# Kernel optimization log

Measured on AMD Instinct MI355X. Metric: run time of the kernel, lower is better.

The kernel has to match this reference:

```python
import jax, jax.numpy as jnp
import numpy as np

CHAIN = (0, 1, 2)
BETA, GAMMA, REG = 1.0, 500.0, 0.2


def _rbf(x, y, V, l):
    """exp(- sum_{V,d}(x-y)^2 / (d*V*V)) + l*I, via the |x|^2+|y|^2-2xy trick.
    x, y: (N, V, d)."""
    N, _, d = x.shape
    xf = x.reshape(N, -1)
    yf = y.reshape(N, -1)
    sq = (jnp.sum(xf * xf, axis=1)[:, None]
          + jnp.sum(yf * yf, axis=1)[None, :]
          - 2.0 * (xf @ yf.T))  # (N, N) sum of squared diffs over V*d
    k = jnp.exp(-sq / (d * V * V))
    if l != 0.0:
        k = k + l * jnp.eye(N, dtype=x.dtype)
    return k


def _trprod(A, B):
    # trace(A @ B) without materializing the product
    return jnp.sum(A * B.T)


def _cmmd(Q, P, endo, exo, l):
    N = Q.shape[0]
    P = jnp.broadcast_to(P, Q.shape)  # handles std_norm with d=1
    endo = list(endo)
    Ve = len(endo)
    qe, pe = Q[:, endo, :], P[:, endo, :]
    Lqq = _rbf(qe, qe, Ve, 0.0)
    Lpp = _rbf(pe, pe, Ve, 0.0)
    Lqp = _rbf(qe, pe, Ve, 0.0)
    if len(exo) == 0:
        # conditional matrices are all-ones -> trace(L @ J) = sum(L)
        return (jnp.sum(Lqq) + jnp.sum(Lpp) - 2.0 * jnp.sum(Lqp)) / (N * N)
    exo = list(exo)
    Vx = len(exo)
    qx, px = Q[:, exo, :], P[:, exo, :]
    Kq_inv = jnp.linalg.inv(_rbf(qx, qx, Vx, l))
    Kp_inv = jnp.linalg.inv(_rbf(px, px, Vx, l))
    Cqq = Kq_inv @ _rbf(qx, qx, Vx, 0.0) @ Kq_inv
    Cpp = Kp_inv @ _rbf(px, px, Vx, 0.0) @ Kp_inv
    Cqp = Kp_inv @ _rbf(px, qx, Vx, 0.0) @ Kq_inv  # inv(Kpp) @ Kpq @ inv(Kqq)
    return (_trprod(Lqq, Cqq) + _trprod(Lpp, Cpp)
            - 2.0 * _trprod(Lqp, Cqp)) / (N * N)


def setup_inputs() -> dict:
    key = jax.random.key(0)
    ks = jax.random.split(key, 5)
    N, V, d, D = 4096, 8, 32, 256
    return {
        "x": jax.random.normal(ks[0], (N, D), dtype=jnp.float32),
        "z": jax.random.normal(ks[1], (N, V, d), dtype=jnp.float32),
        "zz": jax.random.normal(ks[2], (N, V, d), dtype=jnp.float32),
        "xx": jax.random.normal(ks[3], (N, D), dtype=jnp.float32),
        "std_norm": jax.random.normal(ks[4], (N, V, 1), dtype=jnp.float32),
    }


def reference(x, z, zz, xx, std_norm):
    all_endo = tuple(range(z.shape[1]))
    mmd = BETA * _cmmd(z, std_norm, all_endo, (), 0.1)
    mmd = mmd + GAMMA * (
        _cmmd(zz, z, (CHAIN[0],), (CHAIN[1],), REG)
        + _cmmd(zz, z, (CHAIN[1],), (CHAIN[2],), REG)
        + _cmmd(zz, z, (CHAIN[0],), (CHAIN[2],), REG))
    nll = jnp.sum((xx - x) ** 2) / (2.0 * x.shape[0])
    return mmd, nll
```

## Files before the change

### kernel.cpp

```cpp
#include <hip/hip_runtime.h>
#include <math.h>

#define NN 4096
#define DD 256
#define NV 8
#define VD 32
#define NB 128
#define NBLK (NN/NB)
#define NTRI (NBLK*(NBLK+1)/2)

#define RMAP(ty,u) ((ty)*4 + (((u)>>2)<<6) + ((u)&3))
#define CMAP(tx,v) ((tx)*4 + (((v)>>2)<<6) + ((v)&3))

typedef __attribute__((ext_vector_type(8))) short bf16x8;
typedef __attribute__((ext_vector_type(4))) float f32x4;

#define AS1(p) ((const __attribute__((address_space(1))) void*)(p))
#define AS3(p) ((__attribute__((address_space(3))) void*)(p))

__device__ __forceinline__ void stage16(const ushort* g, ushort* l){
  __builtin_amdgcn_global_load_lds(AS1(g), AS3(l), 16, 0, 0);
}

__device__ __forceinline__ ushort f2bf(float x){
  uint u = __float_as_uint(x);
  u += 0x7FFFu + ((u >> 16) & 1u);
  return (ushort)(u >> 16);
}
__device__ __forceinline__ float bf2f(ushort h){ return __uint_as_float(((uint)h) << 16); }

__device__ __forceinline__ void tri_map(int p, int& bi, int& bj){
  int b = (int)((sqrtf(8.0f * (float)p + 1.0f) - 1.0f) * 0.5f);
  while ((b + 1) * (b + 2) / 2 <= p) b++;
  while (b * (b + 1) / 2 > p) b--;
  bi = b; bj = p - b * (b + 1) / 2;
}

__device__ __forceinline__ void block_atomic_add(float v, float* red, float* dst){
  #pragma unroll
  for (int off = 32; off > 0; off >>= 1) v += __shfl_down(v, off, 64);
  const int lane = threadIdx.x & 63;
  const int w = threadIdx.x >> 6;
  if (lane == 0) red[w] = v;
  __syncthreads();
  if (threadIdx.x == 0) atomicAdd(dst, red[0] + red[1] + red[2] + red[3]);
  __syncthreads();
}

#define STAGE_AB(tAp, tBp, kk) do { \
  _Pragma("unroll") \
  for (int p_ = 0; p_ < 2; p_++){ \
    const int row_ = p_*64 + (t >> 2); \
    const int lo_ = row_*32 + sch; \
    stage16(Ah + (size_t)(r0 + row_) * NN + (kk) + sch, (tAp) + lo_); \
    stage16(Bh + (size_t)(c0 + row_) * NN + (kk) + sch, (tBp) + lo_); \
  } } while(0)

#define MFMA_STEP(tAp, tBp) do { \
  bf16x8 ah_[4], bh_[4]; \
  _Pragma("unroll") \
  for (int i_ = 0; i_ < 4; i_++){ \
    ah_[i_] = *(const bf16x8*)&(tAp)[(wr*64 + i_*16 + lm)*32 + quad*8]; \
    bh_[i_] = *(const bf16x8*)&(tBp)[(wc*64 + i_*16 + lm)*32 + quad*8]; \
  } \
  _Pragma("unroll") \
  for (int i_ = 0; i_ < 4; i_++) \
    _Pragma("unroll") \
    for (int j_ = 0; j_ < 4; j_++) \
      acc[i_][j_] = __builtin_amdgcn_mfma_f32_16x16x32_bf16(ah_[i_], bh_[j_], acc[i_][j_], 0, 0, 0); \
  } while(0)

#define PIPE_WAIT_BAR(N) do { \
  asm volatile("s_waitcnt vmcnt(" #N ")" ::: "memory"); \
  __builtin_amdgcn_s_barrier(); \
  } while(0)
#define PIPE_BAR() do { \
  asm volatile("" ::: "memory"); \
  __builtin_amdgcn_s_barrier(); \
  asm volatile("" ::: "memory"); \
  } while(0)

#define PIPE_MAIN_LOOP() do { \
  STAGE_AB(shb + 0*8192, shb + 0*8192 + 4096, 0); \
  STAGE_AB(shb + 1*8192, shb + 1*8192 + 4096, 32); \
  STAGE_AB(shb + 2*8192, shb + 2*8192 + 4096, 64); \
  int cur = 0; \
  _Pragma("unroll 1") \
  for (int step = 0; step < 125; step++){ \
    ushort* tA = shb + cur*8192; ushort* tB = tA + 4096; \
    PIPE_WAIT_BAR(8); \
    MFMA_STEP(tA, tB); \
    PIPE_BAR(); \
    STAGE_AB(tA, tB, (step+3)*32); \
    cur++; if (cur == 3) cur = 0; \
  } \
  { ushort* tA = shb + cur*8192; ushort* tB = tA + 4096; \
    PIPE_WAIT_BAR(8); MFMA_STEP(tA, tB); cur++; if (cur == 3) cur = 0; } \
  { ushort* tA = shb + cur*8192; ushort* tB = tA + 4096; \
    PIPE_WAIT_BAR(4); MFMA_STEP(tA, tB); cur++; if (cur == 3) cur = 0; } \
  { ushort* tA = shb + cur*8192; ushort* tB = tA + 4096; \
    PIPE_WAIT_BAR(0); MFMA_STEP(tA, tB); } \
  } while(0)

__global__ void k_zero(float* p, int n){
  int i = blockIdx.x * blockDim.x + threadIdx.x;
  if (i < n) p[i] = 0.f;
}

__global__ void k_norms(const float* __restrict__ z, const float* __restrict__ zz,
                        const float* __restrict__ stdn,
                        float* __restrict__ stdsq, float* __restrict__ zrs,
                        float* __restrict__ nzz, float* __restrict__ nz8){
  int t = blockIdx.x * blockDim.x + threadIdx.x;
  if (t >= NN * NV) return;
  int i = t / NV, v = t % NV;
  const float* zp  = z  + (size_t)i * DD + v * VD;
  const float* zzp = zz + (size_t)i * DD + v * VD;
  float s1 = 0.f, s2 = 0.f, s2z = 0.f;
  #pragma unroll
  for (int k = 0; k < VD; k++){
    float a = zp[k];  s1 += a; s2 += a * a;
    float b = zzp[k]; s2z += b * b;
  }
  zrs[(size_t)i * NV + v] = s1;
  nz8[(size_t)v * NN + i] = s2;
  nzz[(size_t)v * NN + i] = s2z;
  if (v == 0){
    float s = 0.f;
    #pragma unroll
    for (int u = 0; u < NV; u++){ float a = stdn[(size_t)i * NV + u]; s += a * a; }
    stdsq[i] = s;
  }
}

__global__ void k_rownorm(const float* __restrict__ nz8, float* __restrict__ nrmz){
  int i = blockIdx.x * blockDim.x + threadIdx.x;
  if (i < NN){
    float s = 0.f;
    #pragma unroll
    for (int v = 0; v < NV; v++) s += nz8[(size_t)v * NN + i];
    nrmz[i] = s;
  }
}

__global__ __launch_bounds__(256) void k_nll(const float* __restrict__ x,
                                             const float* __restrict__ xx,
                                             float* __restrict__ slots){
  __shared__ float red[4];
  float s = 0.f;
  const int total = NN * DD;
  for (int i = (blockIdx.x * 256 + threadIdx.x) * 4; i < total; i += gridDim.x * 256 * 4){
    float4 a = *(const float4*)(x + i);
    float4 b = *(const float4*)(xx + i);
    float d0 = b.x - a.x, d1 = b.y - a.y, d2 = b.z - a.z, d3 = b.w - a.w;
    s += d0*d0 + d1*d1 + d2*d2 + d3*d3;
  }
  block_atomic_add(s, red, slots + 3);
}

__global__ __launch_bounds__(256) void k_sqq(const float* __restrict__ z,
                                             const float* __restrict__ nrm,
                                             float* __restrict__ slots){
  __shared__ float Xr[128 * 33];
  __shared__ float Xc[128 * 33];
  __shared__ float red[4];
  int bi, bj; tri_map(blockIdx.x, bi, bj);
  const int r0 = bi * 128, c0 = bj * 128;
  const float wgt = (bi != bj) ? 2.f : 1.f;
  const int t = threadIdx.x;
  const int tx = t & 15, ty = t >> 4;
  const int lrow = t >> 1, lh = t & 1;
  float acc[8][8];
  #pragma unroll
  for (int u = 0; u < 8; u++)
    #pragma unroll
    for (int v = 0; v < 8; v++) acc[u][v] = 0.f;
  for (int ks = 0; ks < DD; ks += 32){
    const float* pr = z + (size_t)(r0 + lrow) * DD + ks + lh * 16;
    const float* pc = z + (size_t)(c0 + lrow) * DD + ks + lh * 16;
    float* dr = &Xr[lrow * 33 + lh * 16];
    float* dc = &Xc[lrow * 33 + lh * 16];
    #pragma unroll
    for (int u = 0; u < 4; u++){
      float4 a = ((const float4*)pr)[u];
      dr[4*u+0] = a.x; dr[4*u+1] = a.y; dr[4*u+2] = a.z; dr[4*u+3] = a.w;
      float4 b = ((const float4*)pc)[u];
      dc[4*u+0] = b.x; dc[4*u+1] = b.y; dc[4*u+2] = b.z; dc[4*u+3] = b.w;
    }
    __syncthreads();
    #pragma unroll
    for (int kk = 0; kk < 32; kk++){
      float a[8], b[8];
      #pragma unroll
      for (int u = 0; u < 8; u++) a[u] = Xr[RMAP(ty,u)*33 + kk];
      #pragma unroll
      for (int v = 0; v < 8; v++) b[v] = Xc[CMAP(tx,v)*33 + kk];
      #pragma unroll
      for (int u = 0; u < 8; u++)
        #pragma unroll
        for (int v = 0; v < 8; v++) acc[u][v] += a[u] * b[v];
    }
    __syncthreads();
  }
  float s = 0.f;
  #pragma unroll 1
  for (int u = 0; u < 8; u++){
    const float ni = nrm[r0 + RMAP(ty,u)];
    #pragma unroll 1
    for (int v = 0; v < 8; v++)
      s += __expf(-(ni + nrm[c0 + CMAP(tx,v)] - 2.f * acc[u][v]) * (1.f/2048.f));
  }
  block_atomic_add(s * wgt, red, slots + 0);
}

__global__ __launch_bounds__(256) void k_spp_sqp(const float* __restrict__ stdn,
                                                 const float* __restrict__ stdsq,
                                                 const float* __restrict__ zrs,
                                                 const float* __restrict__ nrmz,
                                                 float* __restrict__ slots){
  __shared__ float sI[128*9], sJ[128*9], zI[128*9];
  __shared__ float qI[128], qJ[128], nI[128];
  __shared__ float red[4];
  const int r0 = blockIdx.y * 128, c0 = blockIdx.x * 128;
  const int t = threadIdx.x;
  if (t < 128){
    #pragma unroll
    for (int v = 0; v < 8; v++){
      sI[t*9+v] = stdn[(size_t)(r0+t)*NV + v];
      sJ[t*9+v] = stdn[(size_t)(c0+t)*NV + v];
      zI[t*9+v] = zrs[(size_t)(r0+t)*NV + v];
    }
    qI[t] = stdsq[r0+t]; qJ[t] = stdsq[c0+t]; nI[t] = nrmz[r0+t];
  }
  __syncthreads();
  const int tx = t & 15, ty = t >> 4;
  float spp = 0.f, sqp = 0.f;
  #pragma unroll 1
  for (int u = 0; u < 8; u++){
    int i = ty + 16*u;
    #pragma unroll 1
    for (int v = 0; v < 8; v++){
      int j = tx + 16*v;
      float dpp = 0.f, dqp = 0.f;
      #pragma unroll
      for (int k = 0; k < 8; k++){
        float sj = sJ[j*9+k];
        dpp += sI[i*9+k] * sj;
        dqp += zI[i*9+k] * sj;
      }
      spp += __expf(-(qI[i] + qJ[j] - 2.f*dpp) * (1.f/64.f));
      sqp += __expf(-(nI[i] + 32.f*qJ[j] - 2.f*dqp) * (1.f/2048.f));
    }
  }
  block_atomic_add(spp, red, slots + 1);
  block_atomic_add(sqp, red, slots + 2);
}

__global__ __launch_bounds__(256) void k_rbf(const float* __restrict__ Xr_,
                                             const float* __restrict__ Xc_,
                                             const float* __restrict__ nr,
                                             const float* __restrict__ nc,
                                             float lam, float* __restrict__ M){
  __shared__ float Xr[128 * 33];
  __shared__ float Xc[128 * 33];
  const int r0 = blockIdx.y * 128, c0 = blockIdx.x * 128;
  const int t = threadIdx.x;
  const int tx = t & 15, ty = t >> 4;
  const int lrow = t >> 1, lh = t & 1;
  {
    const float* pr = Xr_ + (size_t)(r0 + lrow) * DD + lh * 16;
    const float* pc = Xc_ + (size_t)(c0 + lrow) * DD + lh * 16;
    float* dr = &Xr[lrow * 33 + lh * 16];
    float* dc = &Xc[lrow * 33 + lh * 16];
    #pragma unroll
    for (int u = 0; u < 4; u++){
      float4 a = ((const float4*)pr)[u];
      dr[4*u+0]=a.x; dr[4*u+1]=a.y; dr[4*u+2]=a.z; dr[4*u+3]=a.w;
      float4 b = ((const float4*)pc)[u];
      dc[4*u+0]=b.x; dc[4*u+1]=b.y; dc[4*u+2]=b.z; dc[4*u+3]=b.w;
    }
  }
  __syncthreads();
  #pragma unroll 1
  for (int u = 0; u < 8; u++){
    const int gi = r0 + RMAP(ty,u);
    const float* xi = &Xr[RMAP(ty,u)*33];
    const float ni = nr[gi];
    float vals[8];
    #pragma unroll 1
    for (int v = 0; v < 8; v++){
      const int gj = c0 + CMAP(tx,v);
      const float* xj = &Xc[CMAP(tx,v)*33];
      float d = 0.f;
      #pragma unroll
      for (int k = 0; k < 32; k++) d += xi[k] * xj[k];
      float e = __expf(-(ni + nc[gj] - 2.f*d) * (1.f/32.f));
      if (gi == gj) e += lam;
      vals[v] = e;
    }
    float* pd = M + (size_t)gi * NN + c0 + tx*4;
    *(float4*)pd        = make_float4(vals[0], vals[1], vals[2], vals[3]);
    *(float4*)(pd + 64) = make_float4(vals[4], vals[5], vals[6], vals[7]);
  }
}

__global__ __launch_bounds__(256) void k_rbf16(const float* __restrict__ Xr_,
                                               const float* __restrict__ Xc_,
                                               const float* __restrict__ nr,
                                               const float* __restrict__ nc,
                                               ushort* __restrict__ Mh){
  __shared__ float Xr[128 * 33];
  __shared__ float Xc[128 * 33];
  const int r0 = blockIdx.y * 128, c0 = blockIdx.x * 128;
  const int t = threadIdx.x;
  const int tx = t & 15, ty = t >> 4;
  const int lrow = t >> 1, lh = t & 1;
  {
    const float* pr = Xr_ + (size_t)(r0 + lrow) * DD + lh * 16;
    const float* pc = Xc_ + (size_t)(c0 + lrow) * DD + lh * 16;
    float* dr = &Xr[lrow * 33 + lh * 16];
    float* dc = &Xc[lrow * 33 + lh * 16];
    #pragma unroll
    for (int u = 0; u < 4; u++){
      float4 a = ((const float4*)pr)[u];
      dr[4*u+0]=a.x; dr[4*u+1]=a.y; dr[4*u+2]=a.z; dr[4*u+3]=a.w;
      float4 b = ((const float4*)pc)[u];
      dc[4*u+0]=b.x; dc[4*u+1]=b.y; dc[4*u+2]=b.z; dc[4*u+3]=b.w;
    }
  }
  __syncthreads();
  #pragma unroll 1
  for (int u = 0; u < 8; u++){
    const int gi = r0 + RMAP(ty,u);
    const float* xi = &Xr[RMAP(ty,u)*33];
    const float ni = nr[gi];
    ushort vals[8];
    #pragma unroll 1
    for (int v = 0; v < 8; v++){
      const int gj = c0 + CMAP(tx,v);
      const float* xj = &Xc[CMAP(tx,v)*33];
      float d = 0.f;
      #pragma unroll
      for (int k = 0; k < 32; k++) d += xi[k] * xj[k];
      vals[v] = f2bf(__expf(-(ni + nc[gj] - 2.f*d) * (1.f/32.f)));
    }
    ushort* pd = Mh + (size_t)gi * NN + c0 + tx*4;
    *(ushort4*)pd        = make_ushort4(vals[0], vals[1], vals[2], vals[3]);
    *(ushort4*)(pd + 64) = make_ushort4(vals[4], vals[5], vals[6], vals[7]);
  }
}

__global__ __launch_bounds__(256) void k_split(const float* __restrict__ S,
                                               ushort* __restrict__ H){
  size_t i = ((size_t)blockIdx.x * 256 + threadIdx.x) * 4;
  float4 x = *(const float4*)(S + i);
  *(ushort4*)(H + i) = make_ushort4(f2bf(x.x), f2bf(x.y), f2bf(x.z), f2bf(x.w));
}

__global__ __launch_bounds__(256) void k_mfma_tr(
    const ushort* __restrict__ Ah, const ushort* __restrict__ Bh,
    int sym, int doRed, int nepi,
    const float* e0xr, const float* e0xc, const float* e0nr, const float* e0nc, int s0, int rs0,
    const float* e1xr, const float* e1xc, const float* e1nr, const float* e1nc, int s1, int rs1,
    float* __restrict__ slots){
  __shared__ __align__(16) ushort shb[24576];
  __shared__ float red[4];
  int bi, bj;
  if (sym){
    int p = blockIdx.x;
    p = (p & 7) * (NTRI/8) + (p >> 3);
    tri_map(p, bi, bj);
  } else {
    int id = blockIdx.y * NBLK + blockIdx.x;
    id = (id & 7) * ((NBLK*NBLK)/8) + (id >> 3);
    bi = id / NBLK; bj = id % NBLK;
  }
  const int r0 = bi * 128, c0 = bj * 128;
  const float wgt = (sym && bi != bj) ? 2.f : 1.f;
  const int t = threadIdx.x;
  const int L = t & 63, w = t >> 6;
  const int wr = w >> 1, wc = w & 1;
  const int lm = L & 15, quad = L >> 4;
  const int sch = (t & 3) * 8;

  f32x4 acc[4][4];
  #pragma unroll
  for (int i = 0; i < 4; i++)
    #pragma unroll
    for (int j = 0; j < 4; j++) acc[i][j] = (f32x4){0.f, 0.f, 0.f, 0.f};

  PIPE_MAIN_LOOP();
  __syncthreads();

  #pragma unroll 1
  for (int e = 0; e < nepi; e++){
    const float* xr = e ? e1xr : e0xr;
    const float* xc = e ? e1xc : e0xc;
    const float* nr = e ? e1nr : e0nr;
    const float* nc = e ? e1nc : e0nc;
    const int slot = e ? s1 : s0;
    const int rslot = e ? rs1 : rs0;
    ushort* Xrh = shb;
    ushort* Xrl = shb + 4096;
    ushort* Xch = shb + 8192;
    ushort* Xcl = shb + 12288;
    {
      const int lr = t >> 1, lh = (t & 1) * 16;
      const float* pr = xr + (size_t)(r0 + lr) * DD + lh;
      const float* pc = xc + (size_t)(c0 + lr) * DD + lh;
      ushort* drh = Xrh + lr*32 + lh;  ushort* drl = Xrl + lr*32 + lh;
      ushort* dch = Xch + lr*32 + lh;  ushort* dcl = Xcl + lr*32 + lh;
      #pragma unroll
      for (int u = 0; u < 4; u++){
        float4 a = ((const float4*)pr)[u];
        ushort h0 = f2bf(a.x), h1 = f2bf(a.y), h2 = f2bf(a.z), h3 = f2bf(a.w);
        ((ushort4*)drh)[u] = make_ushort4(h0, h1, h2, h3);
        ((ushort4*)drl)[u] = make_ushort4(f2bf(a.x - bf2f(h0)), f2bf(a.y - bf2f(h1)),
                                          f2bf(a.z - bf2f(h2)), f2bf(a.w - bf2f(h3)));
        float4 b = ((const float4*)pc)[u];
        ushort g0 = f2bf(b.x), g1 = f2bf(b.y), g2 = f2bf(b.z), g3 = f2bf(b.w);
        ((ushort4*)dch)[u] = make_ushort4(g0, g1, g2, g3);
        ((ushort4*)dcl)[u] = make_ushort4(f2bf(b.x - bf2f(g0)), f2bf(b.y - bf2f(g1)),
                                          f2bf(b.z - bf2f(g2)), f2bf(b.w - bf2f(g3)));
      }
    }
    __syncthreads();
    float s = 0.f, s2 = 0.f;
    #pragma unroll 1
    for (int i = 0; i < 4; i++){
      const int ao = (wr*64 + i*16 + lm)*32 + quad*8;
      const bf16x8 ahh = *(const bf16x8*)&Xrh[ao];
      const bf16x8 ahl = *(const bf16x8*)&Xrl[ao];
      f32x4 dj[4];
      #pragma unroll
      for (int j = 0; j < 4; j++){
        const int bo = (wc*64 + j*16 + lm)*32 + quad*8;
        bf16x8 bhh = *(const bf16x8*)&Xch[bo];
        bf16x8 bhl = *(const bf16x8*)&Xcl[bo];
        f32x4 dd = (f32x4){0.f, 0.f, 0.f, 0.f};
        dd = __builtin_amdgcn_mfma_f32_16x16x32_bf16(ahh, bhh, dd, 0, 0, 0);
        dd = __builtin_amdgcn_mfma_f32_16x16x32_bf16(ahl, bhh, dd, 0, 0, 0);
        dd = __builtin_amdgcn_mfma_f32_16x16x32_bf16(ahh, bhl, dd, 0, 0, 0);
        dj[j] = dd;
      }
      #pragma unroll
      for (int rg = 0; rg < 4; rg++){
        const int rl = wr*64 + i*16 + quad*4 + rg;
        const float ni = nr[r0 + rl];
        #pragma unroll
        for (int j = 0; j < 4; j++){
          const int cl = wc*64 + j*16 + lm;
          const float Lval = __expf(-(ni + nc[c0 + cl] - 2.f*dj[j][rg]) * (1.f/32.f));
          s += acc[i][j][rg] * Lval;
          if (doRed) s2 += bf2f(Ah[(size_t)(r0 + rl) * NN + c0 + cl]) * Lval;
        }
      }
    }
    block_atomic_add(s * wgt, red, slots + slot);
    if (doRed) block_atomic_add(s2 * wgt, red, slots + rslot);
    __syncthreads();
  }
}

__global__ __launch_bounds__(256) void k_mfma_gemm(
    const ushort* __restrict__ Ah, const ushort* __restrict__ Bh,
    ushort* __restrict__ Dh){
  __shared__ __align__(16) ushort shb[24576];
  int id = blockIdx.y * NBLK + blockIdx.x;
  id = (id & 7) * ((NBLK*NBLK)/8) + (id >> 3);
  const int r0 = (id / NBLK) * 128, c0 = (id % NBLK) * 128;
  const int t = threadIdx.x;
  const int L = t & 63, w = t >> 6;
  const int wr = w >> 1, wc = w & 1;
  const int lm = L & 15, quad = L >> 4;
  const int sch = (t & 3) * 8;
  f32x4 acc[4][4];
  #pragma unroll
  for (int i = 0; i < 4; i++)
    #pragma unroll
    for (int j = 0; j < 4; j++) acc[i][j] = (f32x4){0.f, 0.f, 0.f, 0.f};
  PIPE_MAIN_LOOP();
  #pragma unroll
  for (int i = 0; i < 4; i++)
    #pragma unroll
    for (int j = 0; j < 4; j++)
      #pragma unroll
      for (int rg = 0; rg < 4; rg++){
        const int row = wr*64 + i*16 + quad*4 + rg;
        const int col = wc*64 + j*16 + lm;
        Dh[(size_t)(r0 + row) * NN + c0 + col] = f2bf(acc[i][j][rg]);
      }
}

__global__ __launch_bounds__(512) void k_gj_diagpanel(
    float* __restrict__ M0, float* __restrict__ M1,
    float* __restrict__ Pbuf, ushort* __restrict__ Pth, ushort* __restrict__ Ptl,
    float* __restrict__ Tf, ushort* __restrict__ Tth, ushort* __restrict__ Ttl,
    ushort* __restrict__ Chh, ushort* __restrict__ Chl, int kb){
  __shared__ float Ps[128 * 132];
  __shared__ __align__(16) float rowbufD[2][2][144];
  __shared__ float colbufD[2][2][128];
  __shared__ float Bs[2][16 * 132];
  const int mat = blockIdx.y;
  float* M = mat ? M1 : M0;
  float* P = Pbuf + (size_t)mat * NB * NB;
  ushort* Ph = Pth + (size_t)mat * NB * NB;
  ushort* Pl = Ptl + (size_t)mat * NB * NB;
  float* Tfm = Tf + (size_t)mat * NB * NN;
  ushort* Th = Tth + (size_t)mat * NN * NB;
  ushort* Tl = Ttl + (size_t)mat * NN * NB;
  ushort* Ch = Chh + (size_t)mat * NN * NB;
  ushort* Cl = Chl + (size_t)mat * NN * NB;
  const int k0 = kb * NB;
  const int t = threadIdx.x;
  {
    const int r = t >> 2, g = t & 3;
    float reg[32];
    const float* mrow = M + (size_t)(k0 + r) * NN + k0 + g*32;
    #pragma unroll
    for (int u = 0; u < 8; u++){
      float4 v = ((const float4*)mrow)[u];
      reg[4*u+0]=v.x; reg[4*u+1]=v.y; reg[4*u+2]=v.z; reg[4*u+3]=v.w;
    }
    if (r < 2){
      #pragma unroll
      for (int u = 0; u < 8; u++)
        *(float4*)&rowbufD[0][r][g*36 + 4*u] =
            make_float4(reg[4*u], reg[4*u+1], reg[4*u+2], reg[4*u+3]);
    }
    if (g == 0){ colbufD[0][0][r] = reg[0]; colbufD[0][1][r] = reg[1]; }
    __syncthreads();
    #pragma unroll 1
    for (int m = 0; m < NB/2; m++){
      const int pj = m & 1, pn = pj ^ 1;
      const int pc0 = 2*m, pc1 = 2*m + 1;
      const int pg = pc0 >> 5;
      const int pe0 = pc0 & 31, pe1 = pc1 & 31;
      const float a  = rowbufD[pj][0][pg*36 + pe0];
      const float b_ = rowbufD[pj][0][pg*36 + pe1];
      const float c_ = rowbufD[pj][1][pg*36 + pe0];
      const float d_ = rowbufD[pj][1][pg*36 + pe1];
      const float rdet = 1.0f / (a*d_ - b_*c_);
      const float i00 =  d_*rdet, i01 = -b_*rdet;
      const float i10 = -c_*rdet, i11 =  a*rdet;
      if (r == pc0 || r == pc1){
        const float m0 = (r == pc0) ? i00 : i10;
        const float m1 = (r == pc0) ? i01 : i11;
        #pragma unroll
        for (int u = 0; u < 8; u++){
          float4 r0v = *(const float4*)&rowbufD[pj][0][g*36 + 4*u];
          float4 r1v = *(const float4*)&rowbufD[pj][1][g*36 + 4*u];
          #pragma unroll
          for (int e = 0; e < 4; e++){
            const int c = g*32 + 4*u + e;
            const float w0 = (e==0)?r0v.x:(e==1)?r0v.y:(e==2)?r0v.z:r0v.w;
            const float w1 = (e==0)?r1v.x:(e==1)?r1v.y:(e==2)?r1v.z:r1v.w;
            float nv = m0*w0 + m1*w1;
            if (c == pc0) nv = (r == pc0) ? i00 : i10;
            if (c == pc1) nv = (r == pc0) ? i01 : i11;
            reg[4*u+e] = nv;
          }
        }
      } else {
        const float w0 = colbufD[pj][0][r], w1 = colbufD[pj][1][r];
        const float f0 = w0*i00 + w1*i10;
        const float f1 = w0*i01 + w1*i11;
        #pragma unroll
        for (int u = 0; u < 8; u++){
          float4 r0v = *(const float4*)&rowbufD[pj][0][g*36 + 4*u];
          float4 r1v = *(const float4*)&rowbufD[pj][1][g*36 + 4*u];
          #pragma unroll
          for (int e = 0; e < 4; e++){
            const int c = g*32 + 4*u + e;
            const float q0 = (e==0)?r0v.x:(e==1)?r0v.y:(e==2)?r0v.z:r0v.w;
            const float q1 = (e==0)?r1v.x:(e==1)?r1v.y:(e==2)?r1v.z:r1v.w;
            float nv = fmaf(-f1, q1, fmaf(-f0, q0, reg[4*u+e]));
            if (c == pc0) nv = -f0;
            if (c == pc1) nv = -f1;
            reg[4*u+e] = nv;
          }
        }
      }
      if (m + 1 < NB/2){
        const int pc0n = pc0 + 2, pc1n = pc1 + 2;
        if (g == (pc0n >> 5)){
          const int pe0n = pc0n & 31, pe1n = pc1n & 31;
          #pragma unroll
          for (int e2 = 0; e2 < 32; e2++){
            if (e2 == pe0n) colbufD[pn][0][r] = reg[e2];
            if (e2 == pe1n) colbufD[pn][1][r] = reg[e2];
          }
        }
        if (r == pc0n || r == pc1n){
          const int k = r & 1;
          #pragma unroll
          for (int u = 0; u < 8; u++)
            *(float4*)&rowbufD[pn][k][g*36 + 4*u] =
                make_float4(reg[4*u], reg[4*u+1], reg[4*u+2], reg[4*u+3]);
        }
      }
      __syncthreads();
    }
    #pragma unroll
    for (int u = 0; u < 8; u++)
      *(float4*)&Ps[r*132 + g*32 + 4*u] =
          make_float4(reg[4*u], reg[4*u+1], reg[4*u+2], reg[4*u+3]);
    if (blockIdx.x == 0){
      #pragma unroll
      for (int u = 0; u < 8; u++)
        *(float4*)&P[r*NB + g*32 + 4*u] =
            make_float4(reg[4*u], reg[4*u+1], reg[4*u+2], reg[4*u+3]);
    }
  }
  __syncthreads();
  if (blockIdx.x == 0){
    const int c = t >> 2, rbp = (t & 3) * 32;
    #pragma unroll
    for (int q4 = 0; q4 < 8; q4++){
      ushort h4[4], l4[4];
      #pragma unroll
      for (int e = 0; e < 4; e++){
        float v = Ps[(rbp + q4*4 + e)*132 + c];
        ushort h = f2bf(v);
        h4[e] = h; l4[e] = f2bf(v - bf2f(h));
      }
      *(ushort4*)(Ph + (size_t)c * NB + rbp + q4*4) = make_ushort4(h4[0], h4[1], h4[2], h4[3]);
      *(ushort4*)(Pl + (size_t)c * NB + rbp + q4*4) = make_ushort4(l4[0], l4[1], l4[2], l4[3]);
    }
  }
  const int half = t >> 8, tt = t & 255;
  const int j0 = blockIdx.x * 256 + half * 128;
  {
    const int row = tt >> 1, hc = (tt & 1) * 64;
    const float* src = M + (size_t)(j0 + row) * NN + k0 + hc;
    ushort* dh = Ch + (size_t)(j0 + row) * NB + hc;
    ushort* dl = Cl + (size_t)(j0 + row) * NB + hc;
    #pragma unroll
    for (int u = 0; u < 16; u++){
      float4 v = ((const float4*)src)[u];
      ushort h0 = f2bf(v.x), h1 = f2bf(v.y), h2 = f2bf(v.z), h3 = f2bf(v.w);
      ((ushort4*)dh)[u] = make_ushort4(h0, h1, h2, h3);
      ((ushort4*)dl)[u] = make_ushort4(f2bf(v.x - bf2f(h0)), f2bf(v.y - bf2f(h1)),
                                       f2bf(v.z - bf2f(h2)), f2bf(v.w - bf2f(h3)));
    }
  }
  const int tx = tt & 15, ty = tt >> 4;
  float* myBs = Bs[half];
  float acc[8][8];
  #pragma unroll
  for (int u = 0; u < 8; u++)
    #pragma unroll
    for (int v = 0; v < 8; v++) acc[u][v] = 0.f;
  for (int ks = 0; ks < NB; ks += 16){
    {
      const int kkl = tt >> 4, c8 = (tt & 15) * 8;
      const float* pb = M + (size_t)(k0 + ks + kkl) * NN + j0 + c8;
      float4 b0 = ((const float4*)pb)[0];
      float4 b1 = ((const float4*)pb)[1];
      *(float4*)&myBs[kkl*132 + c8]     = b0;
      *(float4*)&myBs[kkl*132 + c8 + 4] = b1;
    }
    __syncthreads();
    #pragma unroll
    for (int kk = 0; kk < 16; kk++){
      float a[8], b[8];
      #pragma unroll
      for (int u = 0; u < 8; u++) a[u] = Ps[RMAP(ty,u)*132 + ks + kk];
      float4 b0 = *(const float4*)&myBs[kk*132 + tx*4];
      float4 b1 = *(const float4*)&myBs[kk*132 + tx*4 + 64];
      b[0]=b0.x; b[1]=b0.y; b[2]=b0.z; b[3]=b0.w;
      b[4]=b1.x; b[5]=b1.y; b[6]=b1.z; b[7]=b1.w;
      #pragma unroll
      for (int u = 0; u < 8; u++)
        #pragma unroll
        for (int v = 0; v < 8; v++) acc[u][v] += a[u] * b[v];
    }
    __syncthreads();
  }
  #pragma unroll
  for (int u = 0; u < 8; u++){
    const int rr = RMAP(ty,u);
    float* pd = Tfm + (size_t)rr * NN + j0 + tx*4;
    *(float4*)pd        = make_float4(acc[u][0], acc[u][1], acc[u][2], acc[u][3]);
    *(float4*)(pd + 64) = make_float4(acc[u][4], acc[u][5], acc[u][6], acc[u][7]);
    #pragma unroll
    for (int v = 0; v < 8; v++){
      const int cc = j0 + CMAP(tx,v);
      float val = acc[u][v];
      ushort h = f2bf(val);
      Th[(size_t)cc * NB + rr] = h;
      Tl[(size_t)cc * NB + rr] = f2bf(val - bf2f(h));
    }
  }
}

__global__ __launch_bounds__(256) void k_gj_update(float* __restrict__ M0, float* __restrict__ M1,
    const float* __restrict__ Pbuf,
    const ushort* __restrict__ Pth, const ushort* __restrict__ Ptl,
    const float* __restrict__ Tf,
    const ushort* __restrict__ Tth, const ushort* __restrict__ Ttl,
    const ushort* __restrict__ Chh, const ushort* __restrict__ Chl, int kb){
  __shared__ __align__(16) float shchunk[64 * 132];
  ushort* tAh = (ushort*)shchunk;
  ushort* tAl = tAh + 4096;
  ushort* tBh = tAl + 4096;
  ushort* tBl = tBh + 4096;
  const int mat = blockIdx.z;
  float* M = mat ? M1 : M0;
  const float* P = Pbuf + (size_t)mat * NB * NB;
  const ushort* Ph = Pth + (size_t)mat * NB * NB;
  const ushort* Pl = Ptl + (size_t)mat * NB * NB;
  const float* Tfm = Tf + (size_t)mat * NB * NN;
  const ushort* Th = Tth + (size_t)mat * NN * NB;
  const ushort* Tl = Ttl + (size_t)mat * NN * NB;
  const ushort* Ch = Chh + (size_t)mat * NN * NB;
  const ushort* Cl = Chl + (size_t)mat * NN * NB;
  const int jb = blockIdx.x, ib = blockIdx.y;
  const int k0 = kb * NB, i0 = ib * NB, j0 = jb * NB;
  const int t = threadIdx.x;
  if (ib == kb){
    const int row = t >> 1, half = (t & 1) * 64;
    float* dst = M + (size_t)(k0 + row) * NN + j0 + half;
    if (jb == kb){
      const float* src = P + (size_t)row * NB + half;
      #pragma unroll
      for (int u = 0; u < 16; u++) ((float4*)dst)[u] = ((const float4*)src)[u];
    } else {
      const float* src = Tfm + (size_t)row * NN + j0 + half;
      #pragma unroll
      for (int u = 0; u < 16; u++) ((float4*)dst)[u] = ((const float4*)src)[u];
    }
    return;
  }
  const int L = t & 63, w = t >> 6;
  const int wr = w >> 1, wc = w & 1;
  const int lm = L & 15, quad = L >> 4;
  const int sch = (t & 3) * 8;
  const ushort* Bh = (jb == kb) ? Ph : (Th + (size_t)j0 * NB);
  const ushort* Bl = (jb == kb) ? Pl : (Tl + (size_t)j0 * NB);
  const ushort* Ahp = Ch + (size_t)i0 * NB;
  const ushort* Alp = Cl + (size_t)i0 * NB;
  f32x4 acc[4][4];
  #pragma unroll
  for (int i = 0; i < 4; i++)
    #pragma unroll
    for (int j = 0; j < 4; j++) acc[i][j] = (f32x4){0.f, 0.f, 0.f, 0.f};
  for (int ks = 0; ks < NB; ks += 32){
    #pragma unroll
    for (int p = 0; p < 2; p++){
      const int row = p*64 + (t >> 2);
      const size_t ga = (size_t)row * NB + ks + sch;
      const int lo = row*32 + sch;
      stage16(Ahp + ga, tAh + lo);
      stage16(Alp + ga, tAl + lo);
      stage16(Bh + ga, tBh + lo);
      stage16(Bl + ga, tBl + lo);
    }
    __syncthreads();
    bf16x8 ah[4], al[4], bh[4], bl[4];
    #pragma unroll
    for (int i = 0; i < 4; i++){
      const int ao = (wr*64 + i*16 + lm)*32 + quad*8;
      const int bo = (wc*64 + i*16 + lm)*32 + quad*8;
      ah[i] = *(const bf16x8*)&tAh[ao];
      al[i] = *(const bf16x8*)&tAl[ao];
      bh[i] = *(const bf16x8*)&tBh[bo];
      bl[i] = *(const bf16x8*)&tBl[bo];
    }
    #pragma unroll
    for (int i = 0; i < 4; i++)
      #pragma unroll
      for (int j = 0; j < 4; j++){
        acc[i][j] = __builtin_amdgcn_mfma_f32_16x16x32_bf16(ah[i], bh[j], acc[i][j], 0, 0, 0);
        acc[i][j] = __builtin_amdgcn_mfma_f32_16x16x32_bf16(ah[i], bl[j], acc[i][j], 0, 0, 0);
        acc[i][j] = __builtin_amdgcn_mfma_f32_16x16x32_bf16(al[i], bh[j], acc[i][j], 0, 0, 0);
      }
    __syncthreads();
  }
  const int rloc = t >> 2, cg = (t & 3) * 4;
  const int jc0 = (jb == kb) ? k0 : j0;
  #pragma unroll 1
  for (int hp = 0; hp < 2; hp++){
    if (wr == hp){
      #pragma unroll
      for (int i = 0; i < 4; i++)
        #pragma unroll
        for (int j = 0; j < 4; j++)
          #pragma unroll
          for (int rg = 0; rg < 4; rg++){
            const int row = i*16 + quad*4 + rg;
            const int col = wc*64 + j*16 + lm;
            shchunk[row*132 + col] = acc[i][j][rg];
          }
    }
    __syncthreads();
    float* pm = M + (size_t)(i0 + hp*64 + rloc) * NN + jc0;
    if (jb == kb){
      #pragma unroll
      for (int c = 0; c < 8; c++){
        const int col = cg + 16*c;
        float4 v = *(float4*)&shchunk[rloc*132 + col];
        *(float4*)(pm + col) = make_float4(-v.x, -v.y, -v.z, -v.w);
      }
    } else {
      #pragma unroll
      for (int c = 0; c < 8; c++){
        const int col = cg + 16*c;
        float4 v = *(float4*)&shchunk[rloc*132 + col];
        float4 m = *(float4*)(pm + col);
        m.x -= v.x; m.y -= v.y; m.z -= v.z; m.w -= v.w;
        *(float4*)(pm + col) = m;
      }
    }
    __syncthreads();
  }
}

__global__ void k_combine(const float* __restrict__ slots, float* __restrict__ out){
  if (threadIdx.x == 0 && blockIdx.x == 0){
    const double invN2 = 1.0 / ((double)NN * (double)NN);
    double term1 = ((double)slots[0] + (double)slots[1] - 2.0 * (double)slots[2]) * invN2;
    double pairs = 0.0;
    for (int p = 0; p < 3; p++){
      const float* s = slots + 4 + 5 * p;
      pairs += ((double)s[0] - 0.2 * (double)s[1] + (double)s[2] - 0.2 * (double)s[3] - 2.0 * (double)s[4]);
    }
    out[0] = (float)(1.0 * term1 + 500.0 * pairs * invN2);
    out[1] = (float)((double)slots[3] / (2.0 * (double)NN));
  }
}

extern "C" void kernel_launch(void* const* d_in, const int* in_sizes, int n_in,
                              void* d_out, int out_size, void* d_ws, size_t ws_size,
                              hipStream_t stream){
  const float* x    = (const float*)d_in[0];
  const float* z    = (const float*)d_in[1];
  const float* zz   = (const float*)d_in[2];
  const float* xx   = (const float*)d_in[3];
  const float* stdn = (const float*)d_in[4];
  float* out = (float*)d_out;
  float* ws  = (float*)d_ws;

  const size_t NN2 = (size_t)NN * NN;
  float* R0 = ws;
  float* R1 = R0 + NN2;
  float* R2 = R1 + NN2;
  float* PanelF = R2 + NN2;
  ushort* Tth = (ushort*)PanelF;
  ushort* Ttl = Tth + 2 * (size_t)NB * NN;
  ushort* Chh = Ttl + 2 * (size_t)NB * NN;
  ushort* Chl = Chh + 2 * (size_t)NB * NN;
  float* Tf   = (float*)(Chl + 2 * (size_t)NB * NN);
  float* Pb   = Tf + 2 * (size_t)NB * NN;
  ushort* Pth = (ushort*)(Pb + 2 * (size_t)NB * NB);
  ushort* Ptl = Pth + 2 * (size_t)NB * NB;
  float* slots= (float*)(Ptl + 2 * (size_t)NB * NB);
  float* stdsq= slots + 32;
  float* zrs  = stdsq + NN;
  float* nzz  = zrs + (size_t)NN * NV;
  float* nz8  = nzz + (size_t)NV * NN;
  float* nrmz = nz8 + (size_t)NV * NN;

  ushort* R0h = (ushort*)R0;
  ushort* R2h = (ushort*)R2;
  ushort* Vh  = (ushort*)R1;
  ushort* QPh = Vh + NN2;

  dim3 g32(NBLK, NBLK);

  k_zero<<<1, 64, 0, stream>>>(slots, 32);
  k_norms<<<(NN * NV) / 256, 256, 0, stream>>>(z, zz, stdn, stdsq, zrs, nzz, nz8);
  k_rownorm<<<NN / 256, 256, 0, stream>>>(nz8, nrmz);
  k_nll<<<1024, 256, 0, stream>>>(x, xx, slots);
  k_sqq<<<NTRI, 256, 0, stream>>>(z, nrmz, slots);
  k_spp_sqp<<<g32, 256, 0, stream>>>(stdn, stdsq, zrs, nrmz, slots);

  const float* zz0 = zz;            const float* z0 = z;
  const float* zz1 = zz + VD;       const float* z1 = z + VD;
  const float* nzz0 = nzz;          const float* nz0 = nz8;
  const float* nzz1 = nzz + NN;     const float* nz1 = nz8 + NN;

  for (int b = 1; b <= 2; b++){
    const float* zzb = zz + b*VD;  const float* nzzb = nzz + (size_t)b*NN;
    const float* zb  = z + b*VD;   const float* nzb  = nz8 + (size_t)b*NN;
    k_rbf<<<g32, 256, 0, stream>>>(zzb, zzb, nzzb, nzzb, 0.2f, R0);
    k_rbf<<<g32, 256, 0, stream>>>(zb,  zb,  nzb,  nzb,  0.2f, R1);
    for (int kb = 0; kb < NBLK; kb++){
      k_gj_diagpanel<<<dim3(16, 2), 512, 0, stream>>>(R0, R1, Pb, Pth, Ptl,
                                                      Tf, Tth, Ttl, Chh, Chl, kb);
      k_gj_update<<<dim3(NBLK, NBLK, 2), 256, 0, stream>>>(R0, R1, Pb, Pth, Ptl,
                                                           Tf, Tth, Ttl, Chh, Chl, kb);
    }
    k_split<<<16384, 256, 0, stream>>>(R0, R2h);
    k_split<<<16384, 256, 0, stream>>>(R1, R0h);
    k_rbf16<<<g32, 256, 0, stream>>>(zzb, zb, nzzb, nzb, QPh);
    k_mfma_gemm<<<g32, 256, 0, stream>>>(R0h, QPh, Vh);
    if (b == 1){
      k_mfma_tr<<<NTRI, 256, 0, stream>>>(R2h, R2h, 1, 1, 1,
                                          zz0, zz0, nzz0, nzz0, 5, 4,
                                          nullptr, nullptr, nullptr, nullptr, 0, 0, slots);
      k_mfma_tr<<<NTRI, 256, 0, stream>>>(R0h, R0h, 1, 1, 1,
                                          z0, z0, nz0, nz0, 7, 6,
                                          nullptr, nullptr, nullptr, nullptr, 0, 0, slots);
      k_mfma_tr<<<g32, 256, 0, stream>>>(R2h, Vh, 0, 0, 1,
                                         zz0, z0, nzz0, nz0, 8, 0,
                                         nullptr, nullptr, nullptr, nullptr, 0, 0, slots);
    } else {
      k_mfma_tr<<<NTRI, 256, 0, stream>>>(R2h, R2h, 1, 1, 2,
                                          zz1, zz1, nzz1, nzz1, 10, 9,
                                          zz0, zz0, nzz0, nzz0, 15, 14, slots);
      k_mfma_tr<<<NTRI, 256, 0, stream>>>(R0h, R0h, 1, 1, 2,
                                          z1, z1, nz1, nz1, 12, 11,
                                          z0, z0, nz0, nz0, 17, 16, slots);
      k_mfma_tr<<<g32, 256, 0, stream>>>(R2h, Vh, 0, 0, 2,
                                         zz1, z1, nzz1, nz1, 13, 0,
                                         zz0, z0, nzz0, nz0, 18, 0, slots);
    }
  }
  k_combine<<<1, 1, 0, stream>>>(slots, out);
}
```

Measured before the change: 15.09 ms.

## Pivot eight columns per Gauss-Jordan step in diagonal panel inversion

The diagonal-block Gauss-Jordan inversion now eliminates 8 pivot columns per iteration instead of 2. Each thread inverts the 8x8 pivot block redundantly with a 2x2-block Schur complement built on 4x4 inverses, then applies a rank-8 update. This cuts the serial loop from 64 to 16 iterations, and with it the number of __syncthreads barriers, while raising per-step arithmetic, register pressure and shared memory use. Pivoting without row exchanges over a block of 8 may be slightly less numerically stable.

```diff
diff --git a/kernel.cpp b/kernel.cpp
--- a/kernel.cpp
+++ b/kernel.cpp
@@ -34,6 +34,53 @@
   while ((b + 1) * (b + 2) / 2 <= p) b++;
   while (b * (b + 1) / 2 > p) b--;
   bi = b; bj = p - b * (b + 1) / 2;
+}
+
+__device__ __forceinline__ void inv4(const float A[4][4], float R[4][4]){
+  const float a00=A[0][0], a01=A[0][1], a10=A[1][0], a11=A[1][1];
+  const float b00=A[0][2], b01=A[0][3], b10=A[1][2], b11=A[1][3];
+  const float c00=A[2][0], c01=A[2][1], c10=A[3][0], c11=A[3][1];
+  const float d00=A[2][2], d01=A[2][3], d10=A[3][2], d11=A[3][3];
+  const float rda = 1.0f / (a00*a11 - a01*a10);
+  const float Ai00 =  a11*rda, Ai01 = -a01*rda;
+  const float Ai10 = -a10*rda, Ai11 =  a00*rda;
+  const float CA00 = c00*Ai00 + c01*Ai10, CA01 = c00*Ai01 + c01*Ai11;
+  const float CA10 = c10*Ai00 + c11*Ai10, CA11 = c10*Ai01 + c11*Ai11;
+  const float AB00 = Ai00*b00 + Ai01*b10, AB01 = Ai00*b01 + Ai01*b11;
+  const float AB10 = Ai10*b00 + Ai11*b10, AB11 = Ai10*b01 + Ai11*b11;
+  const float S00 = d00 - (CA00*b00 + CA01*b10);
+  const float S01 = d01 - (CA00*b01 + CA01*b11);
+  const float S10 = d10 - (CA10*b00 + CA11*b10);
+  const float S11 = d11 - (CA10*b01 + CA11*b11);
+  const float rds = 1.0f / (S00*S11 - S01*S10);
+  const float Si00 =  S11*rds, Si01 = -S01*rds;
+  const float Si10 = -S10*rds, Si11 =  S00*rds;
+  const float X00 = AB00*Si00 + AB01*Si10, X01 = AB00*Si01 + AB01*Si11;
+  const float X10 = AB10*Si00 + AB11*Si10, X11 = AB10*Si01 + AB11*Si11;
+  R[0][0] = Ai00 + (X00*CA00 + X01*CA10);
+  R[0][1] = Ai01 + (X00*CA01 + X01*CA11);
+  R[1][0] = Ai10 + (X10*CA00 + X11*CA10);
+  R[1][1] = Ai11 + (X10*CA01 + X11*CA11);
+  R[0][2] = -X00; R[0][3] = -X01;
+  R[1][2] = -X10; R[1][3] = -X11;
+  R[2][0] = -(Si00*CA00 + Si01*CA10);
+  R[2][1] = -(Si00*CA01 + Si01*CA11);
+  R[3][0] = -(Si10*CA00 + Si11*CA10);
+  R[3][1] = -(Si10*CA01 + Si11*CA11);
+  R[2][2] = Si00; R[2][3] = Si01;
+  R[3][2] = Si10; R[3][3] = Si11;
+}
+
+__device__ __forceinline__ void mm4(const float A[4][4], const float B[4][4], float C[4][4]){
+  #pragma unroll
+  for (int i = 0; i < 4; i++)
+    #pragma unroll
+    for (int j = 0; j < 4; j++){
+      float s = 0.f;
+      #pragma unroll
+      for (int k = 0; k < 4; k++) s += A[i][k] * B[k][j];
+      C[i][j] = s;
+    }
 }
 
 __device__ __forceinline__ void block_atomic_add(float v, float* red, float* dst){
@@ -498,8 +545,8 @@
     float* __restrict__ Tf, ushort* __restrict__ Tth, ushort* __restrict__ Ttl,
     ushort* __restrict__ Chh, ushort* __restrict__ Chl, int kb){
   __shared__ float Ps[128 * 132];
-  __shared__ __align__(16) float rowbufD[2][2][144];
-  __shared__ float colbufD[2][2][128];
+  __shared__ __align__(16) float rowbufD[2][8][144];
+  __shared__ float colbufD[2][8][128];
   __shared__ float Bs[2][16 * 132];
   const int mat = blockIdx.y;
   float* M = mat ? M1 : M0;
@@ -522,77 +569,136 @@
       float4 v = ((const float4*)mrow)[u];
       reg[4*u+0]=v.x; reg[4*u+1]=v.y; reg[4*u+2]=v.z; reg[4*u+3]=v.w;
     }
-    if (r < 2){
+    if (r < 8){
       #pragma unroll
       for (int u = 0; u < 8; u++)
         *(float4*)&rowbufD[0][r][g*36 + 4*u] =
             make_float4(reg[4*u], reg[4*u+1], reg[4*u+2], reg[4*u+3]);
     }
-    if (g == 0){ colbufD[0][0][r] = reg[0]; colbufD[0][1][r] = reg[1]; }
+    if (g == 0){
+      #pragma unroll
+      for (int k = 0; k < 8; k++) colbufD[0][k][r] = reg[k];
+    }
     __syncthreads();
     #pragma unroll 1
-    for (int m = 0; m < NB/2; m++){
+    for (int m = 0; m < NB/8; m++){
       const int pj = m & 1, pn = pj ^ 1;
-      const int pc0 = 2*m, pc1 = 2*m + 1;
-      const int pg = pc0 >> 5;
-      const int pe0 = pc0 & 31, pe1 = pc1 & 31;
-      const float a  = rowbufD[pj][0][pg*36 + pe0];
-      const float b_ = rowbufD[pj][0][pg*36 + pe1];
-      const float c_ = rowbufD[pj][1][pg*36 + pe0];
-      const float d_ = rowbufD[pj][1][pg*36 + pe1];
-      const float rdet = 1.0f / (a*d_ - b_*c_);
-      const float i00 =  d_*rdet, i01 = -b_*rdet;
-      const float i10 = -c_*rdet, i11 =  a*rdet;
-      if (r == pc0 || r == pc1){
-        const float m0 = (r == pc0) ? i00 : i10;
-        const float m1 = (r == pc0) ? i01 : i11;
+      const int pc0 = 8*m;
+      const int pg = pc0 >> 5, pe = pc0 & 31;
+      float B8[8][8];
+      #pragma unroll
+      for (int i = 0; i < 8; i++)
+        #pragma unroll
+        for (int j = 0; j < 8; j++)
+          B8[i][j] = rowbufD[pj][i][pg*36 + pe + j];
+      float I8[8][8];
+      {
+        float A4[4][4], B4[4][4], C4[4][4], D4[4][4];
+        #pragma unroll
+        for (int i = 0; i < 4; i++)
+          #pragma unroll
+          for (int j = 0; j < 4; j++){
+            A4[i][j] = B8[i][j];     B4[i][j] = B8[i][j+4];
+            C4[i][j] = B8[i+4][j];   D4[i][j] = B8[i+4][j+4];
+          }
+        float Ai[4][4]; inv4(A4, Ai);
+        float CA[4][4]; mm4(C4, Ai, CA);
+        float AB[4][4]; mm4(Ai, B4, AB);
+        float S4[4][4]; mm4(CA, B4, S4);
+        #pragma unroll
+        for (int i = 0; i < 4; i++)
+          #pragma unroll
+          for (int j = 0; j < 4; j++) S4[i][j] = D4[i][j] - S4[i][j];
+        float Si[4][4]; inv4(S4, Si);
+        float X4[4][4]; mm4(AB, Si, X4);
+        float XC[4][4]; mm4(X4, CA, XC);
+        float LC[4][4]; mm4(Si, CA, LC);
+        #pragma unroll
+        for (int i = 0; i < 4; i++)
+          #pragma unroll
+          for (int j = 0; j < 4; j++){
+            I8[i][j]     = Ai[i][j] + XC[i][j];
+            I8[i][j+4]   = -X4[i][j];
+            I8[i+4][j]   = -LC[i][j];
+            I8[i+4][j+4] = Si[i][j];
+          }
+      }
+      const int rl = r - pc0;
+      if (rl >= 0 && rl < 8){
+        float mk[8];
+        #pragma unroll
+        for (int k = 0; k < 8; k++){
+          float v = I8[0][k];
+          v = (rl==1) ? I8[1][k] : v;
+          v = (rl==2) ? I8[2][k] : v;
+          v = (rl==3) ? I8[3][k] : v;
+          v = (rl==4) ? I8[4][k] : v;
+          v = (rl==5) ? I8[5][k] : v;
+          v = (rl==6) ? I8[6][k] : v;
+          v = (rl==7) ? I8[7][k] : v;
+          mk[k] = v;
+        }
         #pragma unroll
         for (int u = 0; u < 8; u++){
-          float4 r0v = *(const float4*)&rowbufD[pj][0][g*36 + 4*u];
-          float4 r1v = *(const float4*)&rowbufD[pj][1][g*36 + 4*u];
+          float q[8][4];
+          #pragma unroll
+          for (int k = 0; k < 8; k++){
+            float4 rv = *(const float4*)&rowbufD[pj][k][g*36 + 4*u];
+            q[k][0]=rv.x; q[k][1]=rv.y; q[k][2]=rv.z; q[k][3]=rv.w;
+          }
           #pragma unroll
           for (int e = 0; e < 4; e++){
             const int c = g*32 + 4*u + e;
-            const float w0 = (e==0)?r0v.x:(e==1)?r0v.y:(e==2)?r0v.z:r0v.w;
-            const float w1 = (e==0)?r1v.x:(e==1)?r1v.y:(e==2)?r1v.z:r1v.w;
-            float nv = m0*w0 + m1*w1;
-            if (c == pc0) nv = (r == pc0) ? i00 : i10;
-            if (c == pc1) nv = (r == pc0) ? i01 : i11;
+            float nv = 0.f;
+            #pragma unroll
+            for (int k = 0; k < 8; k++) nv = fmaf(mk[k], q[k][e], nv);
+            #pragma unroll
+            for (int k = 0; k < 8; k++) if (c == pc0+k) nv = mk[k];
             reg[4*u+e] = nv;
           }
         }
       } else {
-        const float w0 = colbufD[pj][0][r], w1 = colbufD[pj][1][r];
-        const float f0 = w0*i00 + w1*i10;
-        const float f1 = w0*i01 + w1*i11;
+        float w8[8], f8[8];
+        #pragma unroll
+        for (int k = 0; k < 8; k++) w8[k] = colbufD[pj][k][r];
+        #pragma unroll
+        for (int k = 0; k < 8; k++){
+          float s = 0.f;
+          #pragma unroll
+          for (int i = 0; i < 8; i++) s = fmaf(w8[i], I8[i][k], s);
+          f8[k] = s;
+        }
         #pragma unroll
         for (int u = 0; u < 8; u++){
-          float4 r0v = *(const float4*)&rowbufD[pj][0][g*36 + 4*u];
-          float4 r1v = *(const float4*)&rowbufD[pj][1][g*36 + 4*u];
+          float q[8][4];
+          #pragma unroll
+          for (int k = 0; k < 8; k++){
+            float4 rv = *(const float4*)&rowbufD[pj][k][g*36 + 4*u];
+            q[k][0]=rv.x; q[k][1]=rv.y; q[k][2]=rv.z; q[k][3]=rv.w;
+          }
           #pragma unroll
           for (int e = 0; e < 4; e++){
             const int c = g*32 + 4*u + e;
-            const float q0 = (e==0)?r0v.x:(e==1)?r0v.y:(e==2)?r0v.z:r0v.w;
-            const float q1 = (e==0)?r1v.x:(e==1)?r1v.y:(e==2)?r1v.z:r1v.w;
-            float nv = fmaf(-f1, q1, fmaf(-f0, q0, reg[4*u+e]));
-            if (c == pc0) nv = -f0;
-            if (c == pc1) nv = -f1;
+            float nv = reg[4*u+e];
+            #pragma unroll
+            for (int k = 0; k < 8; k++) nv = fmaf(-f8[k], q[k][e], nv);
+            #pragma unroll
+            for (int k = 0; k < 8; k++) if (c == pc0+k) nv = -f8[k];
             reg[4*u+e] = nv;
           }
         }
       }
-      if (m + 1 < NB/2){
-        const int pc0n = pc0 + 2, pc1n = pc1 + 2;
+      if (m + 1 < NB/8){
+        const int pc0n = pc0 + 8;
         if (g == (pc0n >> 5)){
-          const int pe0n = pc0n & 31, pe1n = pc1n & 31;
+          const int pen = pc0n & 31;
           #pragma unroll
           for (int e2 = 0; e2 < 32; e2++){
-            if (e2 == pe0n) colbufD[pn][0][r] = reg[e2];
-            if (e2 == pe1n) colbufD[pn][1][r] = reg[e2];
+            if (e2 >= pen && e2 < pen + 8) colbufD[pn][e2 - pen][r] = reg[e2];
           }
         }
-        if (r == pc0n || r == pc1n){
-          const int k = r & 1;
+        if (r >= pc0n && r < pc0n + 8){
+          const int k = r - pc0n;
           #pragma unroll
           for (int u = 0; u < 8; u++)
             *(float4*)&rowbufD[pn][k][g*36 + 4*u] =
```

After: 14.98 ms. No clear change (-0.7%).
